# Kernel tuning notes

Measured on AMD Instinct MI355X. Metric: run time of the kernel, lower is better.

## Reference

```python
import jax, jax.numpy as jnp
import numpy as np

N_NODES, N_EDGES = 1024, 4096
D_NODE, D_EDGE, HEADS, N_CLASSES = 128, 256, 4, 16


def setup_inputs() -> dict:
    key = jax.random.key(0)
    ks = jax.random.split(key, 32)
    def w(i, shape):
        return jax.random.normal(ks[i], shape, dtype=jnp.float32) * 0.02
    inp = {
        'node_features': jax.random.normal(ks[0], (N_NODES, D_NODE), dtype=jnp.float32),
        'edge_features': jax.random.normal(ks[1], (N_EDGES, D_EDGE), dtype=jnp.float32),
        'edge_index': jax.random.randint(ks[2], (2, N_EDGES), 0, N_NODES, dtype=jnp.int32),
    }
    i = 3
    for pre in ('a1', 'a2'):
        for nm, shape in [('Wn', (2 * D_NODE, D_EDGE)), ('Wq', (D_EDGE, D_EDGE)),
                          ('Wk', (D_EDGE, D_EDGE)), ('Wv', (D_EDGE, D_EDGE)), ('Wo', (D_EDGE, D_EDGE))]:
            inp[f'{pre}_{nm}'] = w(i, shape); i += 1
            inp[f'{pre}_b{nm[1:].lower()}'] = jnp.zeros((shape[1],), jnp.float32)
    inp['cls_W1'] = w(i, (D_EDGE, D_EDGE)); i += 1
    inp['cls_b1'] = jnp.zeros((D_EDGE,), jnp.float32)
    inp['cls_W2'] = w(i, (D_EDGE, N_CLASSES)); i += 1
    inp['cls_b2'] = jnp.zeros((N_CLASSES,), jnp.float32)
    return inp


def _edge_adjacency(edge_index):
    # edges adjacent iff they share an endpoint (hops=1). [E,E] bool
    src, dst = edge_index[0], edge_index[1]
    return ((src[:, None] == src[None, :]) | (src[:, None] == dst[None, :]) |
            (dst[:, None] == src[None, :]) | (dst[:, None] == dst[None, :]))


def _edge_attention(ef, nf, edge_index, adj, Wn, bn, Wq, bq, Wk, bk, Wv, bv, Wo, bo):
    src, dst = edge_index[0], edge_index[1]
    # gather endpoint node features and fuse into edge representation
    ctx = jnp.concatenate([nf[src], nf[dst]], axis=-1) @ Wn + bn  # [E, D_EDGE]
    x = ef + ctx
    E, D = x.shape
    hd = D // HEADS
    q = (x @ Wq + bq).reshape(E, HEADS, hd)
    k = (x @ Wk + bk).reshape(E, HEADS, hd)
    v = (x @ Wv + bv).reshape(E, HEADS, hd)
    scores = jnp.einsum('ehd,fhd->hef', q, k) / np.float32(np.sqrt(hd))  # [H,E,E]
    scores = jnp.where(adj[None, :, :], scores, jnp.float32(-1e9))
    attn = jax.nn.softmax(scores, axis=-1)
    out = jnp.einsum('hef,fhd->ehd', attn, v).reshape(E, D)
    return x + out @ Wo + bo


def reference(node_features, edge_features, edge_index,
              a1_Wn, a1_bn, a1_Wq, a1_bq, a1_Wk, a1_bk, a1_Wv, a1_bv, a1_Wo, a1_bo,
              a2_Wn, a2_bn, a2_Wq, a2_bq, a2_Wk, a2_bk, a2_Wv, a2_bv, a2_Wo, a2_bo,
              cls_W1, cls_b1, cls_W2, cls_b2):
    adj = _edge_adjacency(edge_index)
    ef = _edge_attention(edge_features, node_features, edge_index, adj,
                         a1_Wn, a1_bn, a1_Wq, a1_bq, a1_Wk, a1_bk, a1_Wv, a1_bv, a1_Wo, a1_bo)
    ef = _edge_attention(ef, node_features, edge_index, adj,
                         a2_Wn, a2_bn, a2_Wq, a2_bq, a2_Wk, a2_bk, a2_Wv, a2_bv, a2_Wo, a2_bo)
    h = jax.nn.gelu(ef @ cls_W1 + cls_b1, approximate=False)
    return h @ cls_W2 + cls_b2
```

## Files before the change

### kernel.cpp

```cpp
#include <hip/hip_runtime.h>
#include <math.h>

#define E_EDGES 4096
#define N_NODES 1024
#define D_NODE 128
#define D_EDGE 256
#define HEADS 4
#define HD 64
#define N_CLASSES 16
#define CAP 128

typedef __attribute__((ext_vector_type(8))) short short8v;
typedef __attribute__((ext_vector_type(4))) float f32x4;

__device__ __forceinline__ unsigned short f2bf(float f) {
    unsigned u = __float_as_uint(f);
    return (unsigned short)((u + 0x7FFFu + ((u >> 16) & 1u)) >> 16);
}
__device__ __forceinline__ float bf2f(unsigned short b) {
    return __uint_as_float(((unsigned)b) << 16);
}

__device__ __forceinline__ void gload_lds16(const void* g, void* l) {
    __builtin_amdgcn_global_load_lds((const __attribute__((address_space(1))) void*)g,
                                     (__attribute__((address_space(3))) void*)l, 16, 0, 0);
}

__device__ __forceinline__ void xcd_remap(int& bx, int& by)
{
    const int nx = gridDim.x;
    const int lid = blockIdx.x + nx * blockIdx.y;
    const int g = lid & 7, s = lid >> 3;
    const int ppx = gridDim.y >> 3;
    by = g * ppx + s / nx;
    bx = s % nx;
}

__global__ __launch_bounds__(256) void prep(
    const float* W0, const float* W1, const float* W2, const float* W3,
    const float* W4, const float* W5, const float* W6, const float* W7,
    const float* W8, const float* W9, const float* W10,
    short* hiT, short* loT,
    const int* __restrict__ src, const int* __restrict__ dst,
    int* __restrict__ cand, int* __restrict__ ccount)
{
    const int t = threadIdx.x;
    if (blockIdx.x < 176) {
        const float* Ws[11] = {W0, W1, W2, W3, W4, W5, W6, W7, W8, W9, W10};
        const int mat = blockIdx.x % 11, byy = blockIdx.x / 11;
        const float* W = Ws[mat];
        short* ho = hiT + (size_t)mat * 65536;
        short* lo = loT + (size_t)mat * 65536;
        const int n = byy * 16 + (t >> 4);
        const int k0 = (t & 15) * 16;
        short8v h0, h1, l0, l1;
#pragma unroll
        for (int j = 0; j < 8; ++j) {
            const float x = W[(size_t)(k0 + j) * 256 + n];
            const unsigned short hb = f2bf(x);
            h0[j] = (short)hb; l0[j] = (short)f2bf(x - bf2f(hb));
        }
#pragma unroll
        for (int j = 0; j < 8; ++j) {
            const float x = W[(size_t)(k0 + 8 + j) * 256 + n];
            const unsigned short hb = f2bf(x);
            h1[j] = (short)hb; l1[j] = (short)f2bf(x - bf2f(hb));
        }
        *(short8v*)&ho[(size_t)n * 256 + k0] = h0;
        *(short8v*)&ho[(size_t)n * 256 + k0 + 8] = h1;
        *(short8v*)&lo[(size_t)n * 256 + k0] = l0;
        *(short8v*)&lo[(size_t)n * 256 + k0 + 8] = l1;
    } else {
        const int w = t >> 6, lane = t & 63;
        const int e = (blockIdx.x - 176) * 4 + w;
        const int a = src[e], b = dst[e];
        int* my = cand + (size_t)e * CAP;
        int base = 0;
        for (int c0 = 0; c0 < E_EDGES; c0 += 64) {
            const int f = c0 + lane;
            const int sf = src[f], df = dst[f];
            const bool adj = (sf == a) | (sf == b) | (df == a) | (df == b);
            const unsigned long long mk = __ballot(adj);
            if (adj) {
                const int pos = base + __popcll(mk & ((1ull << lane) - 1ull));
                if (pos < CAP) my[pos] = f;
            }
            base += __popcll(mk);
        }
        if (lane == 0) ccount[e] = (base < CAP) ? base : CAP;
    }
}

__device__ __forceinline__ void gemm_mfma_core(
    const float* __restrict__ A, const float* __restrict__ A2,
    const short* __restrict__ BhiT, const short* __restrict__ BloT,
    const float* __restrict__ bias, const float* __restrict__ residual,
    const float* __restrict__ residual2, float* __restrict__ C,
    int m0, int n0,
    const float* __restrict__ nf, const int* __restrict__ src,
    const int* __restrict__ dst, int act)
{
    __shared__ short AsH[2][64 * 40];
    __shared__ short AsL[2][64 * 40];
    __shared__ short BsH[2][64 * 32];
    __shared__ short BsL[2][64 * 32];
    const int t = threadIdx.x;
    const int w = t >> 6, lane = t & 63, lr = lane & 15, lg = lane >> 4;
    const int WR = (w >> 1) * 32, WC = (w & 1) * 32;
    const int am = t >> 2, akc = (t & 3) * 8;
    const int bn = t >> 2, bkc = (t & 3) * 8;

    int nS = 0, nD = 0;
    if (nf) { nS = src[m0 + am]; nD = dst[m0 + am]; }

    f32x4 acc00 = {0.f, 0.f, 0.f, 0.f};
    f32x4 acc01 = acc00, acc10 = acc00, acc11 = acc00;
    float4 av0, av1;

#define LOADA_REG(k0)                                                          \
    do {                                                                       \
        const int kq0 = (k0) + akc, kq1 = kq0 + 4;                             \
        if (nf) {                                                              \
            const float* p0 = (kq0 < D_NODE)                                   \
                ? &nf[(size_t)nS * D_NODE + kq0]                               \
                : &nf[(size_t)nD * D_NODE + kq0 - D_NODE];                     \
            const float* p1 = (kq1 < D_NODE)                                   \
                ? &nf[(size_t)nS * D_NODE + kq1]                               \
                : &nf[(size_t)nD * D_NODE + kq1 - D_NODE];                     \
            av0 = *(const float4*)p0; av1 = *(const float4*)p1;                \
        } else {                                                               \
            av0 = *(const float4*)&A[(size_t)(m0 + am) * 256 + kq0];           \
            av1 = *(const float4*)&A[(size_t)(m0 + am) * 256 + kq1];           \
            if (A2) {                                                          \
                const float4 c0_ = *(const float4*)&A2[(size_t)(m0 + am) * 256 + kq0]; \
                const float4 c1_ = *(const float4*)&A2[(size_t)(m0 + am) * 256 + kq1]; \
                av0.x += c0_.x; av0.y += c0_.y; av0.z += c0_.z; av0.w += c0_.w; \
                av1.x += c1_.x; av1.y += c1_.y; av1.z += c1_.z; av1.w += c1_.w; \
            }                                                                  \
        }                                                                      \
    } while (0)
#define SPLIT1(f, j)                                                           \
    { const unsigned short hb = f2bf(f); ah[j] = (short)hb;                    \
      al[j] = (short)f2bf((f) - bf2f(hb)); }
#define STOREA_SPLIT(buf)                                                      \
    do {                                                                       \
        short8v ah, al;                                                        \
        SPLIT1(av0.x, 0) SPLIT1(av0.y, 1) SPLIT1(av0.z, 2) SPLIT1(av0.w, 3)    \
        SPLIT1(av1.x, 4) SPLIT1(av1.y, 5) SPLIT1(av1.z, 6) SPLIT1(av1.w, 7)    \
        *(short8v*)&AsH[buf][am * 40 + akc] = ah;                              \
        *(short8v*)&AsL[buf][am * 40 + akc] = al;                              \
    } while (0)
#define STAGE_B(buf, k0)                                                       \
    do {                                                                       \
        gload_lds16(&BhiT[(size_t)(n0 + bn) * 256 + (k0) + bkc],               \
                    (short*)&BsH[buf][0] + t * 8);                             \
        gload_lds16(&BloT[(size_t)(n0 + bn) * 256 + (k0) + bkc],               \
                    (short*)&BsL[buf][0] + t * 8);                             \
    } while (0)
#define MFMA_STEP(buf)                                                         \
    do {                                                                       \
        const int c0 = WC + lr, c1 = WC + 16 + lr;                             \
        const short8v bH0 = *(const short8v*)&BsH[buf][c0 * 32 + lg * 8];      \
        const short8v bL0 = *(const short8v*)&BsL[buf][c0 * 32 + lg * 8];      \
        const short8v bH1 = *(const short8v*)&BsH[buf][c1 * 32 + lg * 8];      \
        const short8v bL1 = *(const short8v*)&BsL[buf][c1 * 32 + lg * 8];      \
        const short8v aH0 = *(const short8v*)&AsH[buf][(WR + lr) * 40 + lg * 8];      \
        const short8v aL0 = *(const short8v*)&AsL[buf][(WR + lr) * 40 + lg * 8];      \
        const short8v aH1 = *(const short8v*)&AsH[buf][(WR + 16 + lr) * 40 + lg * 8]; \
        const short8v aL1 = *(const short8v*)&AsL[buf][(WR + 16 + lr) * 40 + lg * 8]; \
        acc00 = __builtin_amdgcn_mfma_f32_16x16x32_bf16(aH0, bH0, acc00, 0, 0, 0);    \
        acc01 = __builtin_amdgcn_mfma_f32_16x16x32_bf16(aH0, bH1, acc01, 0, 0, 0);    \
        acc10 = __builtin_amdgcn_mfma_f32_16x16x32_bf16(aH1, bH0, acc10, 0, 0, 0);    \
        acc11 = __builtin_amdgcn_mfma_f32_16x16x32_bf16(aH1, bH1, acc11, 0, 0, 0);    \
        acc00 = __builtin_amdgcn_mfma_f32_16x16x32_bf16(aH0, bL0, acc00, 0, 0, 0);    \
        acc01 = __builtin_amdgcn_mfma_f32_16x16x32_bf16(aH0, bL1, acc01, 0, 0, 0);    \
        acc10 = __builtin_amdgcn_mfma_f32_16x16x32_bf16(aH1, bL0, acc10, 0, 0, 0);    \
        acc11 = __builtin_amdgcn_mfma_f32_16x16x32_bf16(aH1, bL1, acc11, 0, 0, 0);    \
        acc00 = __builtin_amdgcn_mfma_f32_16x16x32_bf16(aL0, bH0, acc00, 0, 0, 0);    \
        acc01 = __builtin_amdgcn_mfma_f32_16x16x32_bf16(aL0, bH1, acc01, 0, 0, 0);    \
        acc10 = __builtin_amdgcn_mfma_f32_16x16x32_bf16(aL1, bH0, acc10, 0, 0, 0);    \
        acc11 = __builtin_amdgcn_mfma_f32_16x16x32_bf16(aL1, bH1, acc11, 0, 0, 0);    \
    } while (0)

    LOADA_REG(0);
    STAGE_B(0, 0);
    STOREA_SPLIT(0);
    __syncthreads();

    for (int kt = 0; kt < 8; ++kt) {
        const int cur = kt & 1;
        if (kt < 7) {
            STAGE_B(cur ^ 1, (kt + 1) * 32);
            LOADA_REG((kt + 1) * 32);
        }
        MFMA_STEP(cur);
        if (kt < 7) STOREA_SPLIT(cur ^ 1);
        __syncthreads();
    }

#define EPI(accv, rt, ct)                                                      \
    do {                                                                       \
        const int col = n0 + WC + (ct) * 16 + lr;                              \
        const float bb = bias ? bias[col] : 0.f;                               \
        _Pragma("unroll") for (int i = 0; i < 4; ++i) {                        \
            const int row = m0 + WR + (rt) * 16 + lg * 4 + i;                  \
            float v = accv[i] + bb;                                            \
            if (residual) v += residual[(size_t)row * D_EDGE + col];           \
            if (residual2) v += residual2[(size_t)row * D_EDGE + col];         \
            if (act == 1) v = 0.5f * v * (1.f + erff(v * 0.70710678118654752f)); \
            C[(size_t)row * D_EDGE + col] = v;                                 \
        }                                                                      \
    } while (0)
    EPI(acc00, 0, 0); EPI(acc01, 0, 1); EPI(acc10, 1, 0); EPI(acc11, 1, 1);
#undef LOADA_REG
#undef SPLIT1
#undef STOREA_SPLIT
#undef STAGE_B
#undef MFMA_STEP
#undef EPI
}

__global__ __launch_bounds__(256) void gemm_ctx(
    const float* __restrict__ nf, const int* __restrict__ src,
    const int* __restrict__ dst, const short* __restrict__ whiT,
    const short* __restrict__ wloT, const float* __restrict__ bn1,
    const float* __restrict__ bn2, float* __restrict__ ctx)
{
    int bx = blockIdx.x, by = blockIdx.y;
    xcd_remap(bx, by);
    const int Lyr = by >> 6, rb = by & 63;
    const short* BH = whiT + (size_t)(Lyr * 5) * 65536;
    const short* BL = wloT + (size_t)(Lyr * 5) * 65536;
    gemm_mfma_core(nullptr, nullptr, BH, BL, Lyr ? bn2 : bn1,
                   nullptr, nullptr, ctx + (size_t)Lyr * E_EDGES * D_EDGE,
                   rb * 64, bx * 64, nf, src, dst, 0);
}

__global__ __launch_bounds__(256) void gemm_mfma(
    const float* __restrict__ A, const float* __restrict__ A2,
    const short* __restrict__ BhiT, const short* __restrict__ BloT,
    const float* __restrict__ bias, const float* __restrict__ residual,
    const float* __restrict__ residual2, float* __restrict__ C, int act)
{
    int bx = blockIdx.x, by = blockIdx.y;
    xcd_remap(bx, by);
    gemm_mfma_core(A, A2, BhiT, BloT, bias, residual, residual2, C,
                   by * 64, bx * 64, nullptr, nullptr, nullptr, act);
}

__global__ __launch_bounds__(256) void gemm_mfma_qkv(
    const float* __restrict__ ef_in, const float* __restrict__ ctx,
    const short* __restrict__ whiT, const short* __restrict__ wloT,
    const float* __restrict__ bq, const float* __restrict__ bk,
    const float* __restrict__ bv,
    float* __restrict__ qb, float* __restrict__ kb, float* __restrict__ vb,
    int wbase)
{
    int bx = blockIdx.x, by = blockIdx.y;
    xcd_remap(bx, by);
    const int wsel = bx >> 2, nt = bx & 3;
    const short* BH = whiT + (size_t)(wbase + 1 + wsel) * 65536;
    const short* BL = wloT + (size_t)(wbase + 1 + wsel) * 65536;
    const float* bias = (wsel == 0) ? bq : (wsel == 1) ? bk : bv;
    float* C = (wsel == 0) ? qb : (wsel == 1) ? kb : vb;
    gemm_mfma_core(ef_in, ctx, BH, BL, bias, nullptr, nullptr, C,
                   by * 64, nt * 64, nullptr, nullptr, nullptr, 0);
}

__global__ __launch_bounds__(256) void attn_sparse3(
    const float* __restrict__ q, const float* __restrict__ k,
    const float* __restrict__ v, const int* __restrict__ cand,
    const int* __restrict__ ccount, float* __restrict__ out)
{
    __shared__ int lc[CAP];
    const int e = blockIdx.x;
    const int t = threadIdx.x, h = t >> 6, lane = t & 63;
    const int g = lane >> 4, il = lane & 15;
    const int m = ccount[e];
    if (t < m) lc[t] = cand[(size_t)e * CAP + t];
    __syncthreads();

    const float4 q4 = *(const float4*)&q[(size_t)e * D_EDGE + h * HD + il * 4];
    float M = -1e30f, L = 0.f;
    float4 O = make_float4(0.f, 0.f, 0.f, 0.f);

    for (int i0 = 0; i0 < m; i0 += 4) {
        const int ci = i0 + g;
        const bool valid = ci < m;
        float4 k4 = make_float4(0.f, 0.f, 0.f, 0.f), v4 = k4;
        if (valid) {
            const int f = lc[ci];
            k4 = *(const float4*)&k[(size_t)f * D_EDGE + h * HD + il * 4];
            v4 = *(const float4*)&v[(size_t)f * D_EDGE + h * HD + il * 4];
        }
        float sc = q4.x * k4.x + q4.y * k4.y + q4.z * k4.z + q4.w * k4.w;
        sc += __shfl_xor(sc, 1);
        sc += __shfl_xor(sc, 2);
        sc += __shfl_xor(sc, 4);
        sc += __shfl_xor(sc, 8);
        const float s_own = valid ? sc * 0.125f : -1e30f;
        const float s0 = __shfl(s_own, 0);
        const float s1 = __shfl(s_own, 16);
        const float s2 = __shfl(s_own, 32);
        const float s3 = __shfl(s_own, 48);
        const float Mn = fmaxf(M, fmaxf(fmaxf(s0, s1), fmaxf(s2, s3)));
        const float alpha = __expf(M - Mn);
        const float p0 = __expf(s0 - Mn), p1 = __expf(s1 - Mn);
        const float p2 = __expf(s2 - Mn), p3 = __expf(s3 - Mn);
        const float p_own = (g == 0) ? p0 : (g == 1) ? p1 : (g == 2) ? p2 : p3;
        O.x = O.x * alpha + p_own * v4.x;
        O.y = O.y * alpha + p_own * v4.y;
        O.z = O.z * alpha + p_own * v4.z;
        O.w = O.w * alpha + p_own * v4.w;
        L = L * alpha + (p0 + p1 + p2 + p3);
        M = Mn;
    }
    O.x += __shfl_xor(O.x, 16); O.y += __shfl_xor(O.y, 16);
    O.z += __shfl_xor(O.z, 16); O.w += __shfl_xor(O.w, 16);
    O.x += __shfl_xor(O.x, 32); O.y += __shfl_xor(O.y, 32);
    O.z += __shfl_xor(O.z, 32); O.w += __shfl_xor(O.w, 32);
    if (lane < 16) {
        const float invL = 1.f / L;
        float4 r = make_float4(O.x * invL, O.y * invL, O.z * invL, O.w * invL);
        *(float4*)&out[(size_t)e * D_EDGE + h * HD + il * 4] = r;
    }
}

__global__ __launch_bounds__(256) void gemm_small(
    const float* __restrict__ A, const float* __restrict__ B,
    const float* __restrict__ bias, float* __restrict__ C, int N, int K)
{
    __shared__ float As[32][68];
    __shared__ float Bs[32][68];
    const int t = threadIdx.x;
    const int tx = t & 15, ty = t >> 4;
    const int m0 = blockIdx.y * 64, n0 = 0;
    const int ar0 = t >> 3, ak0 = (t & 7) * 4;
    const int br0 = t >> 4, nc = (t & 15) * 4;
    float acc[4][4] = {};

    for (int k0 = 0; k0 < K; k0 += 32) {
        float4 a0 = *(const float4*)&A[(size_t)(m0 + ar0) * K + k0 + ak0];
        float4 a1 = *(const float4*)&A[(size_t)(m0 + ar0 + 32) * K + k0 + ak0];
        float4 b0 = make_float4(0.f, 0.f, 0.f, 0.f), b1 = b0;
        if (n0 + nc < N) {
            b0 = *(const float4*)&B[(size_t)(k0 + br0) * N + n0 + nc];
            b1 = *(const float4*)&B[(size_t)(k0 + br0 + 16) * N + n0 + nc];
        }
        As[ak0 + 0][ar0] = a0.x; As[ak0 + 1][ar0] = a0.y;
        As[ak0 + 2][ar0] = a0.z; As[ak0 + 3][ar0] = a0.w;
        As[ak0 + 0][ar0 + 32] = a1.x; As[ak0 + 1][ar0 + 32] = a1.y;
        As[ak0 + 2][ar0 + 32] = a1.z; As[ak0 + 3][ar0 + 32] = a1.w;
        *(float4*)&Bs[br0][nc] = b0; *(float4*)&Bs[br0 + 16][nc] = b1;
        __syncthreads();
#pragma unroll
        for (int kk = 0; kk < 32; ++kk) {
            const float4 av = *(const float4*)&As[kk][ty * 4];
            const float4 bv = *(const float4*)&Bs[kk][tx * 4];
            const float a_[4] = {av.x, av.y, av.z, av.w};
            const float b_[4] = {bv.x, bv.y, bv.z, bv.w};
#pragma unroll
            for (int i = 0; i < 4; ++i)
#pragma unroll
                for (int j = 0; j < 4; ++j) acc[i][j] += a_[i] * b_[j];
        }
        __syncthreads();
    }

#pragma unroll
    for (int i = 0; i < 4; ++i) {
        const int row = m0 + ty * 4 + i;
        const int col = n0 + tx * 4;
        if (col < N) {
            float4 r = make_float4(acc[i][0], acc[i][1], acc[i][2], acc[i][3]);
            const float4 bb = *(const float4*)&bias[col];
            r.x += bb.x; r.y += bb.y; r.z += bb.z; r.w += bb.w;
            *(float4*)&C[(size_t)row * N + col] = r;
        }
    }
}

extern "C" void kernel_launch(void* const* d_in, const int* in_sizes, int n_in,
                              void* d_out, int out_size, void* d_ws, size_t ws_size,
                              hipStream_t stream)
{
    const float* nf = (const float*)d_in[0];
    const float* ef = (const float*)d_in[1];
    const int* ei = (const int*)d_in[2];
    const int* src = ei;
    const int* dst = ei + E_EDGES;

    const float* a_Wn[2] = {(const float*)d_in[3],  (const float*)d_in[13]};
    const float* a_bn[2] = {(const float*)d_in[4],  (const float*)d_in[14]};
    const float* a_Wq[2] = {(const float*)d_in[5],  (const float*)d_in[15]};
    const float* a_bq[2] = {(const float*)d_in[6],  (const float*)d_in[16]};
    const float* a_Wk[2] = {(const float*)d_in[7],  (const float*)d_in[17]};
    const float* a_bk[2] = {(const float*)d_in[8],  (const float*)d_in[18]};
    const float* a_Wv[2] = {(const float*)d_in[9],  (const float*)d_in[19]};
    const float* a_bv[2] = {(const float*)d_in[10], (const float*)d_in[20]};
    const float* a_Wo[2] = {(const float*)d_in[11], (const float*)d_in[21]};
    const float* a_bo[2] = {(const float*)d_in[12], (const float*)d_in[22]};
    const float* cls_W1 = (const float*)d_in[23];
    const float* cls_b1 = (const float*)d_in[24];
    const float* cls_W2 = (const float*)d_in[25];
    const float* cls_b2 = (const float*)d_in[26];

    const size_t buf = (size_t)E_EDGES * D_EDGE;
    float* ws = (float*)d_ws;
    float* ctx1 = ws + 0 * buf;
    float* ctx2 = ws + 1 * buf;
    float* qb   = ws + 2 * buf;
    float* kb   = ws + 3 * buf;
    float* vb   = ws + 4 * buf;
    float* ao   = ws + 5 * buf;
    float* y1   = ws + 6 * buf;
    float* y2   = ctx1;
    float* hb   = qb;
    int* cand   = (int*)(ws + 7 * buf);
    int* ccount = cand + (size_t)E_EDGES * CAP;
    short* whiT = (short*)(ccount + E_EDGES);
    short* wloT = whiT + (size_t)11 * 65536;

    const dim3 gGemm(D_EDGE / 64, E_EDGES / 64);
    const dim3 gCtx(D_EDGE / 64, 2 * E_EDGES / 64);
    const dim3 gQkv(12, E_EDGES / 64);
    const dim3 gCls(1, E_EDGES / 64);

    prep<<<176 + E_EDGES / 4, 256, 0, stream>>>(
        a_Wn[0], a_Wq[0], a_Wk[0], a_Wv[0], a_Wo[0],
        a_Wn[1], a_Wq[1], a_Wk[1], a_Wv[1], a_Wo[1],
        cls_W1, whiT, wloT, src, dst, cand, ccount);

    gemm_ctx<<<gCtx, 256, 0, stream>>>(nf, src, dst, whiT, wloT,
                                       a_bn[0], a_bn[1], ctx1);

    const float* ef_in = ef;
    const float* ctxL[2] = {ctx1, ctx2};
    float* yout[2] = {y1, y2};
    for (int L = 0; L < 2; ++L) {
        const int wbase = L * 5;
        gemm_mfma_qkv<<<gQkv, 256, 0, stream>>>(
            ef_in, ctxL[L], whiT, wloT, a_bq[L], a_bk[L], a_bv[L],
            qb, kb, vb, wbase);
        attn_sparse3<<<E_EDGES, 256, 0, stream>>>(qb, kb, vb, cand, ccount, ao);
        gemm_mfma<<<gGemm, 256, 0, stream>>>(
            ao, nullptr, whiT + (size_t)(wbase + 4) * 65536,
            wloT + (size_t)(wbase + 4) * 65536,
            a_bo[L], ef_in, ctxL[L], yout[L], 0);
        ef_in = yout[L];
    }

    gemm_mfma<<<gGemm, 256, 0, stream>>>(
        y2, nullptr, whiT + (size_t)10 * 65536, wloT + (size_t)10 * 65536,
        cls_b1, nullptr, nullptr, hb, 1);
    gemm_small<<<gCls, 256, 0, stream>>>(hb, cls_W2, cls_b2, (float*)d_out,
                                         N_CLASSES, D_EDGE);
}
```

Before: 151.5 us.

## Fuse classifier GEMMs, coalesce weight prep, restructure sparse attention loop

The weight-prep kernel now stages 64x64 tiles through LDS, so global reads are coalesced instead of strided column reads. The sparse attention kernel has each 16-lane group keep its own online-softmax state and handle two candidates per iteration, then merges the group states at the end, removing the cross-group score broadcasts. The classifier's two GEMMs (W1 with GELU, then W2) are fused into one MFMA kernel that keeps the hidden activations in LDS, dropping a launch and the hidden-buffer round trip. The fused kernel uses 64 blocks with about 84KB of LDS each, which limits parallelism.

```diff
diff --git a/kernel.cpp b/kernel.cpp
--- a/kernel.cpp
+++ b/kernel.cpp
@@ -44,32 +44,40 @@
     const int* __restrict__ src, const int* __restrict__ dst,
     int* __restrict__ cand, int* __restrict__ ccount)
 {
+    __shared__ float tl[64][65];
     const int t = threadIdx.x;
     if (blockIdx.x < 176) {
         const float* Ws[11] = {W0, W1, W2, W3, W4, W5, W6, W7, W8, W9, W10};
-        const int mat = blockIdx.x % 11, byy = blockIdx.x / 11;
+        const int mat = blockIdx.x >> 4, tile = blockIdx.x & 15;
+        const int k0 = (tile >> 2) * 64, n0 = (tile & 3) * 64;
         const float* W = Ws[mat];
+#pragma unroll
+        for (int p = 0; p < 4; ++p) {
+            const int kr = (t >> 4) + p * 16;
+            const int nc = (t & 15) * 4;
+            *(float4*)&tl[kr][nc] = *(const float4*)&W[(size_t)(k0 + kr) * 256 + n0 + nc];
+        }
+        __syncthreads();
+        const int n = t >> 2, ks = (t & 3) * 16;
+        short8v h0, h1, l0, l1;
+#pragma unroll
+        for (int j = 0; j < 8; ++j) {
+            const float x = tl[ks + j][n];
+            const unsigned short hb = f2bf(x);
+            h0[j] = (short)hb; l0[j] = (short)f2bf(x - bf2f(hb));
+        }
+#pragma unroll
+        for (int j = 0; j < 8; ++j) {
+            const float x = tl[ks + 8 + j][n];
+            const unsigned short hb = f2bf(x);
+            h1[j] = (short)hb; l1[j] = (short)f2bf(x - bf2f(hb));
+        }
         short* ho = hiT + (size_t)mat * 65536;
         short* lo = loT + (size_t)mat * 65536;
-        const int n = byy * 16 + (t >> 4);
-        const int k0 = (t & 15) * 16;
-        short8v h0, h1, l0, l1;
-#pragma unroll
-        for (int j = 0; j < 8; ++j) {
-            const float x = W[(size_t)(k0 + j) * 256 + n];
-            const unsigned short hb = f2bf(x);
-            h0[j] = (short)hb; l0[j] = (short)f2bf(x - bf2f(hb));
-        }
-#pragma unroll
-        for (int j = 0; j < 8; ++j) {
-            const float x = W[(size_t)(k0 + 8 + j) * 256 + n];
-            const unsigned short hb = f2bf(x);
-            h1[j] = (short)hb; l1[j] = (short)f2bf(x - bf2f(hb));
-        }
-        *(short8v*)&ho[(size_t)n * 256 + k0] = h0;
-        *(short8v*)&ho[(size_t)n * 256 + k0 + 8] = h1;
-        *(short8v*)&lo[(size_t)n * 256 + k0] = l0;
-        *(short8v*)&lo[(size_t)n * 256 + k0 + 8] = l1;
+        *(short8v*)&ho[(size_t)(n0 + n) * 256 + k0 + ks] = h0;
+        *(short8v*)&ho[(size_t)(n0 + n) * 256 + k0 + ks + 8] = h1;
+        *(short8v*)&lo[(size_t)(n0 + n) * 256 + k0 + ks] = l0;
+        *(short8v*)&lo[(size_t)(n0 + n) * 256 + k0 + ks + 8] = l1;
     } else {
         const int w = t >> 6, lane = t & 63;
         const int e = (blockIdx.x - 176) * 4 + w;
@@ -267,7 +275,7 @@
                    by * 64, nt * 64, nullptr, nullptr, nullptr, 0);
 }
 
-__global__ __launch_bounds__(256) void attn_sparse3(
+__global__ __launch_bounds__(256) void attn_sparse4(
     const float* __restrict__ q, const float* __restrict__ k,
     const float* __restrict__ v, const int* __restrict__ cand,
     const int* __restrict__ ccount, float* __restrict__ out)
@@ -284,41 +292,42 @@
     float M = -1e30f, L = 0.f;
     float4 O = make_float4(0.f, 0.f, 0.f, 0.f);
 
-    for (int i0 = 0; i0 < m; i0 += 4) {
-        const int ci = i0 + g;
-        const bool valid = ci < m;
-        float4 k4 = make_float4(0.f, 0.f, 0.f, 0.f), v4 = k4;
-        if (valid) {
-            const int f = lc[ci];
-            k4 = *(const float4*)&k[(size_t)f * D_EDGE + h * HD + il * 4];
-            v4 = *(const float4*)&v[(size_t)f * D_EDGE + h * HD + il * 4];
-        }
-        float sc = q4.x * k4.x + q4.y * k4.y + q4.z * k4.z + q4.w * k4.w;
-        sc += __shfl_xor(sc, 1);
-        sc += __shfl_xor(sc, 2);
-        sc += __shfl_xor(sc, 4);
-        sc += __shfl_xor(sc, 8);
-        const float s_own = valid ? sc * 0.125f : -1e30f;
-        const float s0 = __shfl(s_own, 0);
-        const float s1 = __shfl(s_own, 16);
-        const float s2 = __shfl(s_own, 32);
-        const float s3 = __shfl(s_own, 48);
-        const float Mn = fmaxf(M, fmaxf(fmaxf(s0, s1), fmaxf(s2, s3)));
-        const float alpha = __expf(M - Mn);
+    for (int i0 = g; i0 < m; i0 += 8) {
+        const int f0 = lc[i0];
+        const bool ok1 = (i0 + 4) < m;
+        const int f1 = ok1 ? lc[i0 + 4] : f0;
+        const float4 k0 = *(const float4*)&k[(size_t)f0 * D_EDGE + h * HD + il * 4];
+        const float4 v0 = *(const float4*)&v[(size_t)f0 * D_EDGE + h * HD + il * 4];
+        const float4 k1 = *(const float4*)&k[(size_t)f1 * D_EDGE + h * HD + il * 4];
+        const float4 v1 = *(const float4*)&v[(size_t)f1 * D_EDGE + h * HD + il * 4];
+        float s0 = q4.x * k0.x + q4.y * k0.y + q4.z * k0.z + q4.w * k0.w;
+        float s1 = q4.x * k1.x + q4.y * k1.y + q4.z * k1.z + q4.w * k1.w;
+        s0 += __shfl_xor(s0, 1); s1 += __shfl_xor(s1, 1);
+        s0 += __shfl_xor(s0, 2); s1 += __shfl_xor(s1, 2);
+        s0 += __shfl_xor(s0, 4); s1 += __shfl_xor(s1, 4);
+        s0 += __shfl_xor(s0, 8); s1 += __shfl_xor(s1, 8);
+        s0 *= 0.125f;
+        s1 = ok1 ? s1 * 0.125f : -1e30f;
+        const float Mn = fmaxf(M, fmaxf(s0, s1));
+        const float al = __expf(M - Mn);
         const float p0 = __expf(s0 - Mn), p1 = __expf(s1 - Mn);
-        const float p2 = __expf(s2 - Mn), p3 = __expf(s3 - Mn);
-        const float p_own = (g == 0) ? p0 : (g == 1) ? p1 : (g == 2) ? p2 : p3;
-        O.x = O.x * alpha + p_own * v4.x;
-        O.y = O.y * alpha + p_own * v4.y;
-        O.z = O.z * alpha + p_own * v4.z;
-        O.w = O.w * alpha + p_own * v4.w;
-        L = L * alpha + (p0 + p1 + p2 + p3);
+        O.x = O.x * al + p0 * v0.x + p1 * v1.x;
+        O.y = O.y * al + p0 * v0.y + p1 * v1.y;
+        O.z = O.z * al + p0 * v0.z + p1 * v1.z;
+        O.w = O.w * al + p0 * v0.w + p1 * v1.w;
+        L = L * al + p0 + p1;
         M = Mn;
     }
+    float Mo = fmaxf(M, __shfl_xor(M, 16));
+    Mo = fmaxf(Mo, __shfl_xor(Mo, 32));
+    const float sc = __expf(M - Mo);
+    O.x *= sc; O.y *= sc; O.z *= sc; O.w *= sc; L *= sc;
     O.x += __shfl_xor(O.x, 16); O.y += __shfl_xor(O.y, 16);
     O.z += __shfl_xor(O.z, 16); O.w += __shfl_xor(O.w, 16);
+    L += __shfl_xor(L, 16);
     O.x += __shfl_xor(O.x, 32); O.y += __shfl_xor(O.y, 32);
     O.z += __shfl_xor(O.z, 32); O.w += __shfl_xor(O.w, 32);
+    L += __shfl_xor(L, 32);
     if (lane < 16) {
         const float invL = 1.f / L;
         float4 r = make_float4(O.x * invL, O.y * invL, O.z * invL, O.w * invL);
@@ -326,57 +335,130 @@
     }
 }
 
-__global__ __launch_bounds__(256) void gemm_small(
-    const float* __restrict__ A, const float* __restrict__ B,
-    const float* __restrict__ bias, float* __restrict__ C, int N, int K)
-{
-    __shared__ float As[32][68];
-    __shared__ float Bs[32][68];
+__global__ __launch_bounds__(256) void gemm_cls(
+    const float* __restrict__ y, const short* __restrict__ BhiT,
+    const short* __restrict__ BloT, const float* __restrict__ b1,
+    const float* __restrict__ W2, const float* __restrict__ b2,
+    float* __restrict__ outp)
+{
+    __shared__ __attribute__((aligned(16))) char smem[86016];
+    short* AsH = (short*)smem;
+    short* AsL = (short*)(smem + 5120);
+    short* BsH = (short*)(smem + 10240);
+    short* BsL = (short*)(smem + 26624);
+    short* hH  = (short*)smem;
+    short* hL  = (short*)(smem + 33792);
+    float* W2s = (float*)(smem + 67584);
+
     const int t = threadIdx.x;
-    const int tx = t & 15, ty = t >> 4;
-    const int m0 = blockIdx.y * 64, n0 = 0;
-    const int ar0 = t >> 3, ak0 = (t & 7) * 4;
-    const int br0 = t >> 4, nc = (t & 15) * 4;
-    float acc[4][4] = {};
-
-    for (int k0 = 0; k0 < K; k0 += 32) {
-        float4 a0 = *(const float4*)&A[(size_t)(m0 + ar0) * K + k0 + ak0];
-        float4 a1 = *(const float4*)&A[(size_t)(m0 + ar0 + 32) * K + k0 + ak0];
-        float4 b0 = make_float4(0.f, 0.f, 0.f, 0.f), b1 = b0;
-        if (n0 + nc < N) {
-            b0 = *(const float4*)&B[(size_t)(k0 + br0) * N + n0 + nc];
-            b1 = *(const float4*)&B[(size_t)(k0 + br0 + 16) * N + n0 + nc];
-        }
-        As[ak0 + 0][ar0] = a0.x; As[ak0 + 1][ar0] = a0.y;
-        As[ak0 + 2][ar0] = a0.z; As[ak0 + 3][ar0] = a0.w;
-        As[ak0 + 0][ar0 + 32] = a1.x; As[ak0 + 1][ar0 + 32] = a1.y;
-        As[ak0 + 2][ar0 + 32] = a1.z; As[ak0 + 3][ar0 + 32] = a1.w;
-        *(float4*)&Bs[br0][nc] = b0; *(float4*)&Bs[br0 + 16][nc] = b1;
+    const int w = t >> 6, lane = t & 63, lr = lane & 15, lg = lane >> 4;
+    const int WR = (w >> 1) * 32, WC = (w & 1) * 32;
+    const int am = t >> 2, akc = (t & 3) * 8;
+    const int m0 = blockIdx.x * 64;
+
+    f32x4 acc[4][2][2];
+#pragma unroll
+    for (int nt = 0; nt < 4; ++nt)
+#pragma unroll
+        for (int rt = 0; rt < 2; ++rt)
+#pragma unroll
+            for (int ct = 0; ct < 2; ++ct) acc[nt][rt][ct] = (f32x4){0.f, 0.f, 0.f, 0.f};
+
+    for (int kt = 0; kt < 8; ++kt) {
+        const int k0 = kt * 32;
+        {
+            const float4 av0 = *(const float4*)&y[(size_t)(m0 + am) * 256 + k0 + akc];
+            const float4 av1 = *(const float4*)&y[(size_t)(m0 + am) * 256 + k0 + akc + 4];
+            short8v ah, al;
+            const float fv[8] = {av0.x, av0.y, av0.z, av0.w, av1.x, av1.y, av1.z, av1.w};
+#pragma unroll
+            for (int j = 0; j < 8; ++j) {
+                const unsigned short hb = f2bf(fv[j]);
+                ah[j] = (short)hb; al[j] = (short)f2bf(fv[j] - bf2f(hb));
+            }
+            *(short8v*)&AsH[am * 40 + akc] = ah;
+            *(short8v*)&AsL[am * 40 + akc] = al;
+        }
+#pragma unroll
+        for (int p = 0; p < 4; ++p) {
+            const int idx = t + 256 * p;
+            const int n = idx >> 2, k8 = (idx & 3) * 8;
+            gload_lds16(&BhiT[(size_t)n * 256 + k0 + k8], BsH + (size_t)idx * 8);
+            gload_lds16(&BloT[(size_t)n * 256 + k0 + k8], BsL + (size_t)idx * 8);
+        }
         __syncthreads();
-#pragma unroll
-        for (int kk = 0; kk < 32; ++kk) {
-            const float4 av = *(const float4*)&As[kk][ty * 4];
-            const float4 bv = *(const float4*)&Bs[kk][tx * 4];
-            const float a_[4] = {av.x, av.y, av.z, av.w};
-            const float b_[4] = {bv.x, bv.y, bv.z, bv.w};
-#pragma unroll
-            for (int i = 0; i < 4; ++i)
-#pragma unroll
-                for (int j = 0; j < 4; ++j) acc[i][j] += a_[i] * b_[j];
+        const short8v aH0 = *(const short8v*)&AsH[(WR + lr) * 40 + lg * 8];
+        const short8v aL0 = *(const short8v*)&AsL[(WR + lr) * 40 + lg * 8];
+        const short8v aH1 = *(const short8v*)&AsH[(WR + 16 + lr) * 40 + lg * 8];
+        const short8v aL1 = *(const short8v*)&AsL[(WR + 16 + lr) * 40 + lg * 8];
+#pragma unroll
+        for (int nt = 0; nt < 4; ++nt) {
+            const int c0 = nt * 64 + WC + lr, c1 = c0 + 16;
+            const short8v bH0 = *(const short8v*)&BsH[c0 * 32 + lg * 8];
+            const short8v bL0 = *(const short8v*)&BsL[c0 * 32 + lg * 8];
+            const short8v bH1 = *(const short8v*)&BsH[c1 * 32 + lg * 8];
+            const short8v bL1 = *(const short8v*)&BsL[c1 * 32 + lg * 8];
+            acc[nt][0][0] = __builtin_amdgcn_mfma_f32_16x16x32_bf16(aH0, bH0, acc[nt][0][0], 0, 0, 0);
+            acc[nt][0][1] = __builtin_amdgcn_mfma_f32_16x16x32_bf16(aH0, bH1, acc[nt][0][1], 0, 0, 0);
+            acc[nt][1][0] = __builtin_amdgcn_mfma_f32_16x16x32_bf16(aH1, bH0, acc[nt][1][0], 0, 0, 0);
+            acc[nt][1][1] = __builtin_amdgcn_mfma_f32_16x16x32_bf16(aH1, bH1, acc[nt][1][1], 0, 0, 0);
+            acc[nt][0][0] = __builtin_amdgcn_mfma_f32_16x16x32_bf16(aH0, bL0, acc[nt][0][0], 0, 0, 0);
+            acc[nt][0][1] = __builtin_amdgcn_mfma_f32_16x16x32_bf16(aH0, bL1, acc[nt][0][1], 0, 0, 0);
+            acc[nt][1][0] = __builtin_amdgcn_mfma_f32_16x16x32_bf16(aH1, bL0, acc[nt][1][0], 0, 0, 0);
+            acc[nt][1][1] = __builtin_amdgcn_mfma_f32_16x16x32_bf16(aH1, bL1, acc[nt][1][1], 0, 0, 0);
+            acc[nt][0][0] = __builtin_amdgcn_mfma_f32_16x16x32_bf16(aL0, bH0, acc[nt][0][0], 0, 0, 0);
+            acc[nt][0][1] = __builtin_amdgcn_mfma_f32_16x16x32_bf16(aL0, bH1, acc[nt][0][1], 0, 0, 0);
+            acc[nt][1][0] = __builtin_amdgcn_mfma_f32_16x16x32_bf16(aL1, bH0, acc[nt][1][0], 0, 0, 0);
+            acc[nt][1][1] = __builtin_amdgcn_mfma_f32_16x16x32_bf16(aL1, bH1, acc[nt][1][1], 0, 0, 0);
         }
         __syncthreads();
     }
 
 #pragma unroll
+    for (int nt = 0; nt < 4; ++nt)
+#pragma unroll
+        for (int rt = 0; rt < 2; ++rt)
+#pragma unroll
+            for (int ct = 0; ct < 2; ++ct) {
+                const int col = nt * 64 + WC + ct * 16 + lr;
+                const float bb = b1[col];
+#pragma unroll
+                for (int i = 0; i < 4; ++i) {
+                    const int row = WR + rt * 16 + lg * 4 + i;
+                    float vv = acc[nt][rt][ct][i] + bb;
+                    vv = 0.5f * vv * (1.f + erff(vv * 0.70710678118654752f));
+                    const unsigned short hb = f2bf(vv);
+                    hH[row * 264 + col] = (short)hb;
+                    hL[row * 264 + col] = (short)f2bf(vv - bf2f(hb));
+                }
+            }
+#pragma unroll
+    for (int p = 0; p < 4; ++p) {
+        const int idx = t + 256 * p;
+        gload_lds16(&W2[(size_t)idx * 4], W2s + (size_t)idx * 4);
+    }
+    __syncthreads();
+
+    f32x4 o = {0.f, 0.f, 0.f, 0.f};
+#pragma unroll
+    for (int kk = 0; kk < 8; ++kk) {
+        const short8v aH = *(const short8v*)&hH[(w * 16 + lr) * 264 + kk * 32 + lg * 8];
+        const short8v aL = *(const short8v*)&hL[(w * 16 + lr) * 264 + kk * 32 + lg * 8];
+        short8v bH, bL;
+#pragma unroll
+        for (int j = 0; j < 8; ++j) {
+            const float x = W2s[(size_t)(kk * 32 + lg * 8 + j) * 16 + lr];
+            const unsigned short hb = f2bf(x);
+            bH[j] = (short)hb; bL[j] = (short)f2bf(x - bf2f(hb));
+        }
+        o = __builtin_amdgcn_mfma_f32_16x16x32_bf16(aH, bH, o, 0, 0, 0);
+        o = __builtin_amdgcn_mfma_f32_16x16x32_bf16(aH, bL, o, 0, 0, 0);
+        o = __builtin_amdgcn_mfma_f32_16x16x32_bf16(aL, bH, o, 0, 0, 0);
+    }
+#pragma unroll
     for (int i = 0; i < 4; ++i) {
-        const int row = m0 + ty * 4 + i;
-        const int col = n0 + tx * 4;
-        if (col < N) {
-            float4 r = make_float4(acc[i][0], acc[i][1], acc[i][2], acc[i][3]);
-            const float4 bb = *(const float4*)&bias[col];
-            r.x += bb.x; r.y += bb.y; r.z += bb.z; r.w += bb.w;
-            *(float4*)&C[(size_t)row * N + col] = r;
-        }
+        const int row = m0 + w * 16 + lg * 4 + i;
+        outp[(size_t)row * 16 + lr] = o[i] + b2[lr];
     }
 }
 
@@ -415,7 +497,6 @@
     float* ao   = ws + 5 * buf;
     float* y1   = ws + 6 * buf;
     float* y2   = ctx1;
-    float* hb   = qb;
     int* cand   = (int*)(ws + 7 * buf);
     int* ccount = cand + (size_t)E_EDGES * CAP;
     short* whiT = (short*)(ccount + E_EDGES);
@@ -424,7 +505,6 @@
     const dim3 gGemm(D_EDGE / 64, E_EDGES / 64);
     const dim3 gCtx(D_EDGE / 64, 2 * E_EDGES / 64);
     const dim3 gQkv(12, E_EDGES / 64);
-    const dim3 gCls(1, E_EDGES / 64);
 
     prep<<<176 + E_EDGES / 4, 256, 0, stream>>>(
         a_Wn[0], a_Wq[0], a_Wk[0], a_Wv[0], a_Wo[0],
@@ -442,7 +522,7 @@
         gemm_mfma_qkv<<<gQkv, 256, 0, stream>>>(
             ef_in, ctxL[L], whiT, wloT, a_bq[L], a_bk[L], a_bv[L],
             qb, kb, vb, wbase);
-        attn_sparse3<<<E_EDGES, 256, 0, stream>>>(qb, kb, vb, cand, ccount, ao);
+        attn_sparse4<<<E_EDGES, 256, 0, stream>>>(qb, kb, vb, cand, ccount, ao);
         gemm_mfma<<<gGemm, 256, 0, stream>>>(
             ao, nullptr, whiT + (size_t)(wbase + 4) * 65536,
             wloT + (size_t)(wbase + 4) * 65536,
@@ -450,9 +530,7 @@
         ef_in = yout[L];
     }
 
-    gemm_mfma<<<gGemm, 256, 0, stream>>>(
-        y2, nullptr, whiT + (size_t)10 * 65536, wloT + (size_t)10 * 65536,
-        cls_b1, nullptr, nullptr, hb, 1);
-    gemm_small<<<gCls, 256, 0, stream>>>(hb, cls_W2, cls_b2, (float*)d_out,
-                                         N_CLASSES, D_EDGE);
-}
+    gemm_cls<<<64, 256, 0, stream>>>(y2, whiT + (size_t)10 * 65536,
+                                     wloT + (size_t)10 * 65536,
+                                     cls_b1, cls_W2, cls_b2, (float*)d_out);
+}
```

Result: no change. 148.8 us (-1.8%).
